# Optimization experiments

Measured on AMD Instinct MI355X. Metric: run time of the kernel, lower is better.

## Reference

```python
import jax, jax.numpy as jnp
import numpy as np

B = 8192        # batch of spots
T = 137         # target_length: number of predict heads
D = 384         # fea_size(256) + img_size(128)
K = 128         # hidden width of each head
EPS = 1e-5      # BatchNorm1d eps
SLOPE = 0.01    # LeakyReLU negative slope (torch default)


def setup_inputs() -> dict:
    key = jax.random.key(0)
    ks = jax.random.split(key, 5)
    return {
        "f":        jax.random.normal(ks[0], (B, D), dtype=jnp.float32),
        "W1":       jax.random.normal(ks[1], (T, K, D), dtype=jnp.float32) * (1.0 / np.sqrt(D)),
        "b1":       jax.random.normal(ks[2], (T, K), dtype=jnp.float32) * 0.02,
        "gamma":    jnp.ones((T, K), dtype=jnp.float32),
        "beta":     jnp.zeros((T, K), dtype=jnp.float32),
        "run_mean": jnp.zeros((T, K), dtype=jnp.float32),
        "run_var":  jnp.ones((T, K), dtype=jnp.float32),
        "W2":       jax.random.normal(ks[3], (T, K), dtype=jnp.float32) * (1.0 / np.sqrt(K)),
        "b2":       jax.random.normal(ks[4], (T,), dtype=jnp.float32) * 0.02,
    }


def reference(f, W1, b1, gamma, beta, run_mean, run_var, W2, b2):
    # Batched equivalent of: for i in range(137): Linear(384->128)+BN+LeakyReLU+Linear(128->1)
    # all applied to the same feature f; outputs concatenated -> [B, 137].
    h = jnp.einsum('bd,tkd->btk', f, W1) + b1                       # [B, T, K]
    scale = gamma * jax.lax.rsqrt(run_var + EPS)                     # eval-mode BN, [T, K]
    h = (h - run_mean) * scale + beta
    h = jnp.where(h >= 0, h, SLOPE * h)                              # LeakyReLU
    out = jnp.einsum('btk,tk->bt', h, W2) + b2                       # [B, T]
    return out
```

## Files before the change

### kernel.cpp

```cpp
#include <hip/hip_runtime.h>
#include <hip/hip_bf16.h>

constexpr int BATCH = 8192;
constexpr int THEADS = 137;
constexpr int DFEA = 384;
constexpr int KHID = 128;
constexpr float EPS_BN = 1e-5f;
constexpr float SLOPE = 0.01f;

constexpr size_t N_F  = (size_t)BATCH * DFEA;
constexpr size_t N_W1 = (size_t)THEADS * KHID * DFEA;
constexpr size_t WS_NEED = (N_F + N_W1) * sizeof(__hip_bfloat16);
constexpr int C_F8 = (int)(N_F / 8);
constexpr int C_T8 = (int)((N_F + N_W1) / 8);

typedef __attribute__((ext_vector_type(8))) short bf16x8;
typedef __attribute__((ext_vector_type(4))) float f32x4;

__device__ __forceinline__ short cvt_bf16(float x) {
    __hip_bfloat16 b = __float2bfloat16(x);
    return *(short*)&b;
}

__device__ __forceinline__ bf16x8 load8_cvt(const float* __restrict__ g) {
    f32x4 lo = *(const f32x4*)g;
    f32x4 hi = *(const f32x4*)(g + 4);
    bf16x8 r;
    r[0] = cvt_bf16(lo[0]); r[1] = cvt_bf16(lo[1]);
    r[2] = cvt_bf16(lo[2]); r[3] = cvt_bf16(lo[3]);
    r[4] = cvt_bf16(hi[0]); r[5] = cvt_bf16(hi[1]);
    r[6] = cvt_bf16(hi[2]); r[7] = cvt_bf16(hi[3]);
    return r;
}

__device__ __forceinline__ void gload16(const void* g, void* s) {
    __builtin_amdgcn_global_load_lds((const __attribute__((address_space(1))) void*)g,
                                     (__attribute__((address_space(3))) void*)s,
                                     16, 0, 0);
}

__global__ __launch_bounds__(256) void cvt_pass(const float* __restrict__ f,
                                                const float* __restrict__ W1,
                                                __hip_bfloat16* __restrict__ ws) {
    int i = blockIdx.x * 256 + threadIdx.x;
    if (i < C_F8)
        *(bf16x8*)(ws + (size_t)i * 8) = load8_cvt(f + (size_t)i * 8);
    else if (i < C_T8)
        *(bf16x8*)(ws + (size_t)i * 8) = load8_cvt(W1 + ((size_t)i - C_F8) * 8);
}

__global__ __launch_bounds__(256, 2) void fused_heads_bf16(
    const __hip_bfloat16* __restrict__ fb,
    const __hip_bfloat16* __restrict__ W1b,
    const float* __restrict__ b1,
    const float* __restrict__ gmm,
    const float* __restrict__ bta,
    const float* __restrict__ rmean,
    const float* __restrict__ rvar,
    const float* __restrict__ W2,
    const float* __restrict__ b2,
    float* __restrict__ out)
{
    __shared__ __attribute__((aligned(16))) __hip_bfloat16 As[256 * 32];
    __shared__ __attribute__((aligned(16))) __hip_bfloat16 Bs[128 * 32];

    const int tid  = threadIdx.x;
    const int lane = tid & 63;
    const int wm   = tid >> 6;
    const int m0 = blockIdx.x * 256;
    const int t  = blockIdx.y;
    const int n0 = t * KHID;

    const int row16 = lane & 15;
    const int quad  = lane >> 4;
    const int swz   = quad ^ ((row16 >> 1) & 3);

    const __hip_bfloat16* gA[4];
    const __hip_bfloat16* gB[2];
    #pragma unroll
    for (int c = 0; c < 4; ++c) {
        const int li = tid + c * 256;
        const int r = li >> 2, cb = (li & 3) ^ ((li >> 3) & 3);
        gA[c] = fb + (size_t)(m0 + r) * DFEA + cb * 8;
    }
    #pragma unroll
    for (int c = 0; c < 2; ++c) {
        const int li = tid + c * 256;
        const int r = li >> 2, cb = (li & 3) ^ ((li >> 3) & 3);
        gB[c] = W1b + (size_t)(n0 + r) * DFEA + cb * 8;
    }

    f32x4 acc[4][8];
    #pragma unroll
    for (int i = 0; i < 4; ++i)
        #pragma unroll
        for (int j = 0; j < 8; ++j)
            acc[i][j] = (f32x4){0.f, 0.f, 0.f, 0.f};

    #pragma unroll 1
    for (int kt = 0; kt < DFEA / 32; ++kt) {
        const int k0 = kt * 32;
        #pragma unroll
        for (int c = 0; c < 4; ++c)
            gload16(gA[c] + k0, &As[(tid + c * 256) * 8]);
        #pragma unroll
        for (int c = 0; c < 2; ++c)
            gload16(gB[c] + k0, &Bs[(tid + c * 256) * 8]);
        __syncthreads();

        bf16x8 af[4], bfr[8];
        #pragma unroll
        for (int ai = 0; ai < 4; ++ai)
            af[ai] = *(const bf16x8*)&As[(wm * 64 + ai * 16 + row16) * 32 + swz * 8];
        #pragma unroll
        for (int bi = 0; bi < 8; ++bi)
            bfr[bi] = *(const bf16x8*)&Bs[(bi * 16 + row16) * 32 + swz * 8];

        #pragma unroll
        for (int ai = 0; ai < 4; ++ai)
            #pragma unroll
            for (int bi = 0; bi < 8; ++bi)
                acc[ai][bi] = __builtin_amdgcn_mfma_f32_16x16x32_bf16(
                    af[ai], bfr[bi], acc[ai][bi], 0, 0, 0);
        __syncthreads();
    }

    float s[8], cc[8], w2v[8];
    #pragma unroll
    for (int bi = 0; bi < 8; ++bi) {
        const int n = n0 + bi * 16 + row16;
        const float sv = gmm[n] * rsqrtf(rvar[n] + EPS_BN);
        s[bi]   = sv;
        cc[bi]  = bta[n] + (b1[n] - rmean[n]) * sv;
        w2v[bi] = W2[n];
    }

    float p[4][4];
    #pragma unroll
    for (int ai = 0; ai < 4; ++ai)
        #pragma unroll
        for (int r = 0; r < 4; ++r) {
            float a = 0.f;
            #pragma unroll
            for (int bi = 0; bi < 8; ++bi) {
                float y = acc[ai][bi][r] * s[bi] + cc[bi];
                y = (y >= 0.f) ? y : SLOPE * y;
                a += y * w2v[bi];
            }
            p[ai][r] = a;
        }

    #pragma unroll
    for (int mask = 1; mask <= 8; mask <<= 1)
        #pragma unroll
        for (int ai = 0; ai < 4; ++ai)
            #pragma unroll
            for (int r = 0; r < 4; ++r)
                p[ai][r] += __shfl_xor(p[ai][r], mask);

    if (row16 == 0) {
        const float bias = b2[t];
        #pragma unroll
        for (int ai = 0; ai < 4; ++ai)
            #pragma unroll
            for (int r = 0; r < 4; ++r) {
                const int row = m0 + wm * 64 + ai * 16 + quad * 4 + r;
                out[(size_t)row * THEADS + t] = p[ai][r] + bias;
            }
    }
}

__global__ __launch_bounds__(256) void fused_heads_f32(
    const float* __restrict__ f, const float* __restrict__ W1,
    const float* __restrict__ b1, const float* __restrict__ gmm,
    const float* __restrict__ bta, const float* __restrict__ rmean,
    const float* __restrict__ rvar, const float* __restrict__ W2,
    const float* __restrict__ b2, float* __restrict__ out)
{
    __shared__ __attribute__((aligned(16))) __hip_bfloat16 As[128 * 32];
    __shared__ __attribute__((aligned(16))) __hip_bfloat16 Bs[128 * 32];
    __shared__ float red[2][128];

    const int tid  = threadIdx.x;
    const int lane = tid & 63;
    const int wave = tid >> 6;
    const int wm = wave >> 1, wn = wave & 1;
    const int m0 = blockIdx.x * 128;
    const int t  = blockIdx.y;
    const int n0 = t * KHID;

    const int li0 = tid, li1 = tid + 256;
    const int r0 = li0 >> 2, c0 = (li0 & 3) * 8;
    const int r1 = li1 >> 2, c1 = (li1 & 3) * 8;
    const float* gA0 = f  + (size_t)(m0 + r0) * DFEA + c0;
    const float* gA1 = f  + (size_t)(m0 + r1) * DFEA + c1;
    const float* gB0 = W1 + (size_t)(n0 + r0) * DFEA + c0;
    const float* gB1 = W1 + (size_t)(n0 + r1) * DFEA + c1;

    const int row16 = lane & 15, quad = lane >> 4;

    f32x4 acc[4][4];
    #pragma unroll
    for (int i = 0; i < 4; ++i)
        #pragma unroll
        for (int j = 0; j < 4; ++j)
            acc[i][j] = (f32x4){0.f, 0.f, 0.f, 0.f};

    #pragma unroll 1
    for (int kt = 0; kt < DFEA / 32; ++kt) {
        const int k0 = kt * 32;
        bf16x8 va0 = load8_cvt(gA0 + k0);
        bf16x8 va1 = load8_cvt(gA1 + k0);
        bf16x8 vb0 = load8_cvt(gB0 + k0);
        bf16x8 vb1 = load8_cvt(gB1 + k0);
        __syncthreads();
        *(bf16x8*)&As[li0 * 8] = va0;
        *(bf16x8*)&As[li1 * 8] = va1;
        *(bf16x8*)&Bs[li0 * 8] = vb0;
        *(bf16x8*)&Bs[li1 * 8] = vb1;
        __syncthreads();

        bf16x8 af[4], bfr[4];
        #pragma unroll
        for (int i = 0; i < 4; ++i)
            af[i] = *(const bf16x8*)&As[(wm * 64 + i * 16 + row16) * 32 + quad * 8];
        #pragma unroll
        for (int i = 0; i < 4; ++i)
            bfr[i] = *(const bf16x8*)&Bs[(wn * 64 + i * 16 + row16) * 32 + quad * 8];
        #pragma unroll
        for (int ai = 0; ai < 4; ++ai)
            #pragma unroll
            for (int bi = 0; bi < 4; ++bi)
                acc[ai][bi] = __builtin_amdgcn_mfma_f32_16x16x32_bf16(
                    af[ai], bfr[bi], acc[ai][bi], 0, 0, 0);
    }

    float s[4], cc[4], w2v[4];
    #pragma unroll
    for (int bi = 0; bi < 4; ++bi) {
        const int n = n0 + wn * 64 + bi * 16 + row16;
        const float sv = gmm[n] * rsqrtf(rvar[n] + EPS_BN);
        s[bi] = sv;
        cc[bi] = bta[n] + (b1[n] - rmean[n]) * sv;
        w2v[bi] = W2[n];
    }
    float p[4][4];
    #pragma unroll
    for (int ai = 0; ai < 4; ++ai)
        #pragma unroll
        for (int r = 0; r < 4; ++r) {
            float a = 0.f;
            #pragma unroll
            for (int bi = 0; bi < 4; ++bi) {
                float y = acc[ai][bi][r] * s[bi] + cc[bi];
                y = (y >= 0.f) ? y : SLOPE * y;
                a += y * w2v[bi];
            }
            p[ai][r] = a;
        }
    #pragma unroll
    for (int mask = 1; mask <= 8; mask <<= 1)
        #pragma unroll
        for (int ai = 0; ai < 4; ++ai)
            #pragma unroll
            for (int r = 0; r < 4; ++r)
                p[ai][r] += __shfl_xor(p[ai][r], mask);
    if (row16 == 0) {
        #pragma unroll
        for (int ai = 0; ai < 4; ++ai)
            #pragma unroll
            for (int r = 0; r < 4; ++r)
                red[wn][wm * 64 + ai * 16 + quad * 4 + r] = p[ai][r];
    }
    __syncthreads();
    if (tid < 128)
        out[(size_t)(m0 + tid) * THEADS + t] = red[0][tid] + red[1][tid] + b2[t];
}

extern "C" void kernel_launch(void* const* d_in, const int* in_sizes, int n_in,
                              void* d_out, int out_size, void* d_ws, size_t ws_size,
                              hipStream_t stream) {
    (void)in_sizes; (void)n_in; (void)out_size;
    const float* f     = (const float*)d_in[0];
    const float* W1    = (const float*)d_in[1];
    const float* b1    = (const float*)d_in[2];
    const float* gmm   = (const float*)d_in[3];
    const float* bta   = (const float*)d_in[4];
    const float* rmean = (const float*)d_in[5];
    const float* rvar  = (const float*)d_in[6];
    const float* W2    = (const float*)d_in[7];
    const float* b2    = (const float*)d_in[8];
    float* out = (float*)d_out;

    if (ws_size >= WS_NEED) {
        __hip_bfloat16* fb  = (__hip_bfloat16*)d_ws;
        __hip_bfloat16* W1b = fb + N_F;
        cvt_pass<<<(C_T8 + 255) / 256, 256, 0, stream>>>(f, W1, fb);
        dim3 grid(BATCH / 256, THEADS);
        fused_heads_bf16<<<grid, 256, 0, stream>>>(fb, W1b, b1, gmm, bta, rmean, rvar, W2, b2, out);
    } else {
        dim3 grid(BATCH / 128, THEADS);
        fused_heads_f32<<<grid, 256, 0, stream>>>(f, W1, b1, gmm, bta, rmean, rvar, W2, b2, out);
    }
}
```

Measured before the change: 222.0 us.

## Restructure bf16 heads kernel: 512-row tiles, direct A loads, double-buffered W1 chunks

The bf16 fused-heads kernel now uses 512-thread blocks covering 512 batch rows per head. The activation fragments are loaded straight from global memory into registers, skipping LDS. Each head's W1 slice is staged in two 128-wide K chunks with an XOR swizzle and double buffering, and the 1D grid is remapped so neighbouring blocks share heads for L2 reuse. The aim is to cut LDS traffic and barriers per K step and to raise MFMA density. The cost is that uncoalesced per-lane global A loads may stall the MFMA pipeline, and the larger LDS footprint (64KB per block) limits occupancy.

New measurement: 244.6 us. 1.1x slower.

```diff
diff --git a/kernel.cpp b/kernel.cpp
--- a/kernel.cpp
+++ b/kernel.cpp
@@ -13,6 +13,9 @@
 constexpr size_t WS_NEED = (N_F + N_W1) * sizeof(__hip_bfloat16);
 constexpr int C_F8 = (int)(N_F / 8);
 constexpr int C_T8 = (int)((N_F + N_W1) / 8);
+
+constexpr int BM   = 512;
+constexpr int NBLK = (BATCH / BM) * THEADS;
 
 typedef __attribute__((ext_vector_type(8))) short bf16x8;
 typedef __attribute__((ext_vector_type(4))) float f32x4;
@@ -49,7 +52,7 @@
         *(bf16x8*)(ws + (size_t)i * 8) = load8_cvt(W1 + ((size_t)i - C_F8) * 8);
 }
 
-__global__ __launch_bounds__(256, 2) void fused_heads_bf16(
+__global__ __launch_bounds__(512, 2) void fused_heads_v2(
     const __hip_bfloat16* __restrict__ fb,
     const __hip_bfloat16* __restrict__ W1b,
     const float* __restrict__ b1,
@@ -61,76 +64,93 @@
     const float* __restrict__ b2,
     float* __restrict__ out)
 {
-    __shared__ __attribute__((aligned(16))) __hip_bfloat16 As[256 * 32];
-    __shared__ __attribute__((aligned(16))) __hip_bfloat16 Bs[128 * 32];
-
-    const int tid  = threadIdx.x;
-    const int lane = tid & 63;
-    const int wm   = tid >> 6;
-    const int m0 = blockIdx.x * 256;
-    const int t  = blockIdx.y;
-    const int n0 = t * KHID;
-
+    __shared__ __attribute__((aligned(16))) __hip_bfloat16 Bs[2][KHID * 128];
+
+    const int tid   = threadIdx.x;
+    const int lane  = tid & 63;
+    const int wm    = tid >> 6;
     const int row16 = lane & 15;
     const int quad  = lane >> 4;
-    const int swz   = quad ^ ((row16 >> 1) & 3);
+
+    const int bid  = blockIdx.x;
+    const int j    = bid >> 3;
+    const int mblk = ((bid & 7) << 1) | (j & 1);
+    const int t    = j >> 1;
+    const int m0   = mblk * BM;
+    const int n0   = t * KHID;
+
+    const __hip_bfloat16* gB[4];
+    int ldst[4];
+    #pragma unroll
+    for (int jj = 0; jj < 4; ++jj) {
+        const int li = tid + jj * 512;
+        const int r = li >> 4, s = li & 15;
+        gB[jj]   = W1b + (size_t)(n0 + r) * DFEA + ((s ^ (r & 7)) << 3);
+        ldst[jj] = li << 3;
+    }
 
     const __hip_bfloat16* gA[4];
-    const __hip_bfloat16* gB[2];
-    #pragma unroll
-    for (int c = 0; c < 4; ++c) {
-        const int li = tid + c * 256;
-        const int r = li >> 2, cb = (li & 3) ^ ((li >> 3) & 3);
-        gA[c] = fb + (size_t)(m0 + r) * DFEA + cb * 8;
-    }
-    #pragma unroll
-    for (int c = 0; c < 2; ++c) {
-        const int li = tid + c * 256;
-        const int r = li >> 2, cb = (li & 3) ^ ((li >> 3) & 3);
-        gB[c] = W1b + (size_t)(n0 + r) * DFEA + cb * 8;
-    }
+    #pragma unroll
+    for (int ai = 0; ai < 4; ++ai)
+        gA[ai] = fb + (size_t)(m0 + wm * 64 + ai * 16 + row16) * DFEA + quad * 8;
 
     f32x4 acc[4][8];
     #pragma unroll
     for (int i = 0; i < 4; ++i)
         #pragma unroll
-        for (int j = 0; j < 8; ++j)
-            acc[i][j] = (f32x4){0.f, 0.f, 0.f, 0.f};
-
-    #pragma unroll 1
-    for (int kt = 0; kt < DFEA / 32; ++kt) {
-        const int k0 = kt * 32;
-        #pragma unroll
-        for (int c = 0; c < 4; ++c)
-            gload16(gA[c] + k0, &As[(tid + c * 256) * 8]);
-        #pragma unroll
-        for (int c = 0; c < 2; ++c)
-            gload16(gB[c] + k0, &Bs[(tid + c * 256) * 8]);
-        __syncthreads();
-
-        bf16x8 af[4], bfr[8];
-        #pragma unroll
-        for (int ai = 0; ai < 4; ++ai)
-            af[ai] = *(const bf16x8*)&As[(wm * 64 + ai * 16 + row16) * 32 + swz * 8];
-        #pragma unroll
-        for (int bi = 0; bi < 8; ++bi)
-            bfr[bi] = *(const bf16x8*)&Bs[(bi * 16 + row16) * 32 + swz * 8];
-
-        #pragma unroll
-        for (int ai = 0; ai < 4; ++ai)
-            #pragma unroll
-            for (int bi = 0; bi < 8; ++bi)
-                acc[ai][bi] = __builtin_amdgcn_mfma_f32_16x16x32_bf16(
-                    af[ai], bfr[bi], acc[ai][bi], 0, 0, 0);
-        __syncthreads();
-    }
-
-    float s[8], cc[8], w2v[8];
+        for (int jx = 0; jx < 8; ++jx)
+            acc[i][jx] = (f32x4){0.f, 0.f, 0.f, 0.f};
+
+    #pragma unroll
+    for (int jj = 0; jj < 4; ++jj) gload16(gB[jj],       &Bs[0][ldst[jj]]);
+    #pragma unroll
+    for (int jj = 0; jj < 4; ++jj) gload16(gB[jj] + 128, &Bs[1][ldst[jj]]);
+
+    bf16x8 af0[4];
+    #pragma unroll
+    for (int ai = 0; ai < 4; ++ai) af0[ai] = *(const bf16x8*)gA[ai];
+
+    __syncthreads();
+
+#define CHUNK(BUF, C, PRE)                                                   \
+    {                                                                        \
+        _Pragma("unroll")                                                    \
+        for (int ktl = 0; ktl < 4; ++ktl) {                                  \
+            bf16x8 af[4], bfr[8];                                            \
+            _Pragma("unroll")                                                \
+            for (int ai = 0; ai < 4; ++ai)                                   \
+                af[ai] = ((PRE) && ktl == 0) ? af0[ai]                       \
+                       : *(const bf16x8*)(gA[ai] + (C) * 128 + ktl * 32);    \
+            _Pragma("unroll")                                                \
+            for (int bi = 0; bi < 8; ++bi) {                                 \
+                const int rr = bi * 16 + row16;                              \
+                const int ss = (ktl * 4 + quad) ^ (row16 & 7);               \
+                bfr[bi] = *(const bf16x8*)&Bs[BUF][rr * 128 + ss * 8];       \
+            }                                                                \
+            _Pragma("unroll")                                                \
+            for (int ai = 0; ai < 4; ++ai)                                   \
+                _Pragma("unroll")                                            \
+                for (int bi = 0; bi < 8; ++bi)                               \
+                    acc[ai][bi] = __builtin_amdgcn_mfma_f32_16x16x32_bf16(   \
+                        af[ai], bfr[bi], acc[ai][bi], 0, 0, 0);              \
+        }                                                                    \
+    }
+
+    CHUNK(0, 0, true)
+    __syncthreads();
+    #pragma unroll
+    for (int jj = 0; jj < 4; ++jj) gload16(gB[jj] + 256, &Bs[0][ldst[jj]]);
+    CHUNK(1, 1, false)
+    __syncthreads();
+    CHUNK(0, 2, false)
+#undef CHUNK
+
+    float sc[8], cc[8], w2v[8];
     #pragma unroll
     for (int bi = 0; bi < 8; ++bi) {
         const int n = n0 + bi * 16 + row16;
         const float sv = gmm[n] * rsqrtf(rvar[n] + EPS_BN);
-        s[bi]   = sv;
+        sc[bi]  = sv;
         cc[bi]  = bta[n] + (b1[n] - rmean[n]) * sv;
         w2v[bi] = W2[n];
     }
@@ -143,7 +163,7 @@
             float a = 0.f;
             #pragma unroll
             for (int bi = 0; bi < 8; ++bi) {
-                float y = acc[ai][bi][r] * s[bi] + cc[bi];
+                float y = acc[ai][bi][r] * sc[bi] + cc[bi];
                 y = (y >= 0.f) ? y : SLOPE * y;
                 a += y * w2v[bi];
             }
@@ -184,7 +204,7 @@
     const int tid  = threadIdx.x;
     const int lane = tid & 63;
     const int wave = tid >> 6;
-    const int wm = wave >> 1, wn = wave & 1;
+    const int wmv = wave >> 1, wn = wave & 1;
     const int m0 = blockIdx.x * 128;
     const int t  = blockIdx.y;
     const int n0 = t * KHID;
@@ -203,8 +223,8 @@
     #pragma unroll
     for (int i = 0; i < 4; ++i)
         #pragma unroll
-        for (int j = 0; j < 4; ++j)
-            acc[i][j] = (f32x4){0.f, 0.f, 0.f, 0.f};
+        for (int jx = 0; jx < 4; ++jx)
+            acc[i][jx] = (f32x4){0.f, 0.f, 0.f, 0.f};
 
     #pragma unroll 1
     for (int kt = 0; kt < DFEA / 32; ++kt) {
@@ -223,7 +243,7 @@
         bf16x8 af[4], bfr[4];
         #pragma unroll
         for (int i = 0; i < 4; ++i)
-            af[i] = *(const bf16x8*)&As[(wm * 64 + i * 16 + row16) * 32 + quad * 8];
+            af[i] = *(const bf16x8*)&As[(wmv * 64 + i * 16 + row16) * 32 + quad * 8];
         #pragma unroll
         for (int i = 0; i < 4; ++i)
             bfr[i] = *(const bf16x8*)&Bs[(wn * 64 + i * 16 + row16) * 32 + quad * 8];
@@ -270,7 +290,7 @@
         for (int ai = 0; ai < 4; ++ai)
             #pragma unroll
             for (int r = 0; r < 4; ++r)
-                red[wn][wm * 64 + ai * 16 + quad * 4 + r] = p[ai][r];
+                red[wn][wmv * 64 + ai * 16 + quad * 4 + r] = p[ai][r];
     }
     __syncthreads();
     if (tid < 128)
@@ -296,8 +316,7 @@
         __hip_bfloat16* fb  = (__hip_bfloat16*)d_ws;
         __hip_bfloat16* W1b = fb + N_F;
         cvt_pass<<<(C_T8 + 255) / 256, 256, 0, stream>>>(f, W1, fb);
-        dim3 grid(BATCH / 256, THEADS);
-        fused_heads_bf16<<<grid, 256, 0, stream>>>(fb, W1b, b1, gmm, bta, rmean, rvar, W2, b2, out);
+        fused_heads_v2<<<dim3(NBLK), 512, 0, stream>>>(fb, W1b, b1, gmm, bta, rmean, rvar, W2, b2, out);
     } else {
         dim3 grid(BATCH / 128, THEADS);
         fused_heads_f32<<<grid, 256, 0, stream>>>(f, W1, b1, gmm, bta, rmean, rvar, W2, b2, out);
```

## Double-buffer LDS tiles with async prefetch of next K-slice in bf16 kernel

Applied to the files above, without the earlier changes.

The bf16 GEMM loop now uses two LDS buffers for A and B. It issues the global-to-LDS loads for the next K tile before computing on the current one, and uses explicit vmcnt waits and raw barriers instead of two __syncthreads per iteration. This is meant to hide global load latency behind the MFMA work and to cut barrier stalls. It also raises wave priority around the MFMA block. LDS use doubles to 48KB per block, which may limit occupancy at 2 blocks per CU, and the hand-written waitcnt counts must match the number of loads issued.

Result: no change. 223.1 us (+0.5%).

```diff
diff --git a/kernel.cpp b/kernel.cpp
--- a/kernel.cpp
+++ b/kernel.cpp
@@ -49,7 +49,7 @@
         *(bf16x8*)(ws + (size_t)i * 8) = load8_cvt(W1 + ((size_t)i - C_F8) * 8);
 }
 
-__global__ __launch_bounds__(256, 2) void fused_heads_bf16(
+__global__ __launch_bounds__(256, 2) void fused_heads_v5(
     const __hip_bfloat16* __restrict__ fb,
     const __hip_bfloat16* __restrict__ W1b,
     const float* __restrict__ b1,
@@ -61,8 +61,8 @@
     const float* __restrict__ b2,
     float* __restrict__ out)
 {
-    __shared__ __attribute__((aligned(16))) __hip_bfloat16 As[256 * 32];
-    __shared__ __attribute__((aligned(16))) __hip_bfloat16 Bs[128 * 32];
+    __shared__ __attribute__((aligned(16))) __hip_bfloat16 As[2][256 * 32];
+    __shared__ __attribute__((aligned(16))) __hip_bfloat16 Bs[2][128 * 32];
 
     const int tid  = threadIdx.x;
     const int lane = tid & 63;
@@ -97,33 +97,50 @@
         for (int j = 0; j < 8; ++j)
             acc[i][j] = (f32x4){0.f, 0.f, 0.f, 0.f};
 
-    #pragma unroll 1
+#define STAGE(BUF, K0)                                                      \
+    {                                                                       \
+        _Pragma("unroll")                                                   \
+        for (int c = 0; c < 4; ++c)                                         \
+            gload16(gA[c] + (K0), &As[BUF][(tid + c * 256) * 8]);           \
+        _Pragma("unroll")                                                   \
+        for (int c = 0; c < 2; ++c)                                         \
+            gload16(gB[c] + (K0), &Bs[BUF][(tid + c * 256) * 8]);           \
+    }
+
+    STAGE(0, 0);
+
+    #pragma unroll 2
     for (int kt = 0; kt < DFEA / 32; ++kt) {
-        const int k0 = kt * 32;
-        #pragma unroll
-        for (int c = 0; c < 4; ++c)
-            gload16(gA[c] + k0, &As[(tid + c * 256) * 8]);
-        #pragma unroll
-        for (int c = 0; c < 2; ++c)
-            gload16(gB[c] + k0, &Bs[(tid + c * 256) * 8]);
-        __syncthreads();
+        const int cur = kt & 1;
+        if (kt < 11) {
+            STAGE(cur ^ 1, (kt + 1) * 32);
+            asm volatile("s_waitcnt vmcnt(6)" ::: "memory");
+        } else {
+            asm volatile("s_waitcnt vmcnt(0)" ::: "memory");
+        }
+        __builtin_amdgcn_s_barrier();
+        __builtin_amdgcn_sched_barrier(0);
 
         bf16x8 af[4], bfr[8];
         #pragma unroll
         for (int ai = 0; ai < 4; ++ai)
-            af[ai] = *(const bf16x8*)&As[(wm * 64 + ai * 16 + row16) * 32 + swz * 8];
+            af[ai] = *(const bf16x8*)&As[cur][(wm * 64 + ai * 16 + row16) * 32 + swz * 8];
         #pragma unroll
         for (int bi = 0; bi < 8; ++bi)
-            bfr[bi] = *(const bf16x8*)&Bs[(bi * 16 + row16) * 32 + swz * 8];
-
+            bfr[bi] = *(const bf16x8*)&Bs[cur][(bi * 16 + row16) * 32 + swz * 8];
+
+        __builtin_amdgcn_s_setprio(1);
         #pragma unroll
         for (int ai = 0; ai < 4; ++ai)
             #pragma unroll
             for (int bi = 0; bi < 8; ++bi)
                 acc[ai][bi] = __builtin_amdgcn_mfma_f32_16x16x32_bf16(
                     af[ai], bfr[bi], acc[ai][bi], 0, 0, 0);
-        __syncthreads();
-    }
+        __builtin_amdgcn_s_setprio(0);
+
+        __builtin_amdgcn_s_barrier();
+    }
+#undef STAGE
 
     float s[8], cc[8], w2v[8];
     #pragma unroll
@@ -184,7 +201,7 @@
     const int tid  = threadIdx.x;
     const int lane = tid & 63;
     const int wave = tid >> 6;
-    const int wm = wave >> 1, wn = wave & 1;
+    const int wmv = wave >> 1, wn = wave & 1;
     const int m0 = blockIdx.x * 128;
     const int t  = blockIdx.y;
     const int n0 = t * KHID;
@@ -203,8 +220,8 @@
     #pragma unroll
     for (int i = 0; i < 4; ++i)
         #pragma unroll
-        for (int j = 0; j < 4; ++j)
-            acc[i][j] = (f32x4){0.f, 0.f, 0.f, 0.f};
+        for (int jx = 0; jx < 4; ++jx)
+            acc[i][jx] = (f32x4){0.f, 0.f, 0.f, 0.f};
 
     #pragma unroll 1
     for (int kt = 0; kt < DFEA / 32; ++kt) {
@@ -223,7 +240,7 @@
         bf16x8 af[4], bfr[4];
         #pragma unroll
         for (int i = 0; i < 4; ++i)
-            af[i] = *(const bf16x8*)&As[(wm * 64 + i * 16 + row16) * 32 + quad * 8];
+            af[i] = *(const bf16x8*)&As[(wmv * 64 + i * 16 + row16) * 32 + quad * 8];
         #pragma unroll
         for (int i = 0; i < 4; ++i)
             bfr[i] = *(const bf16x8*)&Bs[(wn * 64 + i * 16 + row16) * 32 + quad * 8];
@@ -270,7 +287,7 @@
         for (int ai = 0; ai < 4; ++ai)
             #pragma unroll
             for (int r = 0; r < 4; ++r)
-                red[wn][wm * 64 + ai * 16 + quad * 4 + r] = p[ai][r];
+                red[wn][wmv * 64 + ai * 16 + quad * 4 + r] = p[ai][r];
     }
     __syncthreads();
     if (tid < 128)
@@ -297,7 +314,7 @@
         __hip_bfloat16* W1b = fb + N_F;
         cvt_pass<<<(C_T8 + 255) / 256, 256, 0, stream>>>(f, W1, fb);
         dim3 grid(BATCH / 256, THEADS);
-        fused_heads_bf16<<<grid, 256, 0, stream>>>(fb, W1b, b1, gmm, bta, rmean, rvar, W2, b2, out);
+        fused_heads_v5<<<grid, 256, 0, stream>>>(fb, W1b, b1, gmm, bta, rmean, rvar, W2, b2, out);
     } else {
         dim3 grid(BATCH / 128, THEADS);
         fused_heads_f32<<<grid, 256, 0, stream>>>(f, W1, b1, gmm, bta, rmean, rvar, W2, b2, out);
```

## Load MFMA operands directly from global into registers with double buffering

Applied to the files above, without the earlier changes.

The bf16 GEMM kernel no longer stages A and B tiles through LDS with global_load_lds and two barriers per k-step. Each wave now loads its MFMA fragments straight from global memory into registers, double-buffered across two k-slices in a fully unrolled loop. MFMA blocks run at raised wave priority via s_setprio. This removes LDS traffic and block-wide syncs, but each wave fetches the whole B tile on its own (4x redundant B reads served by cache) and register pressure rises from the two fragment buffers.

Result: slower. 388.5 us (+75.0%).

```diff
diff --git a/kernel.cpp b/kernel.cpp
--- a/kernel.cpp
+++ b/kernel.cpp
@@ -33,12 +33,6 @@
     return r;
 }
 
-__device__ __forceinline__ void gload16(const void* g, void* s) {
-    __builtin_amdgcn_global_load_lds((const __attribute__((address_space(1))) void*)g,
-                                     (__attribute__((address_space(3))) void*)s,
-                                     16, 0, 0);
-}
-
 __global__ __launch_bounds__(256) void cvt_pass(const float* __restrict__ f,
                                                 const float* __restrict__ W1,
                                                 __hip_bfloat16* __restrict__ ws) {
@@ -49,7 +43,7 @@
         *(bf16x8*)(ws + (size_t)i * 8) = load8_cvt(W1 + ((size_t)i - C_F8) * 8);
 }
 
-__global__ __launch_bounds__(256, 2) void fused_heads_bf16(
+__global__ __launch_bounds__(256, 2) void fused_heads_v6(
     const __hip_bfloat16* __restrict__ fb,
     const __hip_bfloat16* __restrict__ W1b,
     const float* __restrict__ b1,
@@ -61,34 +55,51 @@
     const float* __restrict__ b2,
     float* __restrict__ out)
 {
-    __shared__ __attribute__((aligned(16))) __hip_bfloat16 As[256 * 32];
-    __shared__ __attribute__((aligned(16))) __hip_bfloat16 Bs[128 * 32];
-
-    const int tid  = threadIdx.x;
-    const int lane = tid & 63;
-    const int wm   = tid >> 6;
+    const int tid   = threadIdx.x;
+    const int lane  = tid & 63;
+    const int wm    = tid >> 6;
+    const int row16 = lane & 15;
+    const int quad  = lane >> 4;
     const int m0 = blockIdx.x * 256;
     const int t  = blockIdx.y;
     const int n0 = t * KHID;
 
-    const int row16 = lane & 15;
-    const int quad  = lane >> 4;
-    const int swz   = quad ^ ((row16 >> 1) & 3);
-
-    const __hip_bfloat16* gA[4];
-    const __hip_bfloat16* gB[2];
-    #pragma unroll
-    for (int c = 0; c < 4; ++c) {
-        const int li = tid + c * 256;
-        const int r = li >> 2, cb = (li & 3) ^ ((li >> 3) & 3);
-        gA[c] = fb + (size_t)(m0 + r) * DFEA + cb * 8;
-    }
-    #pragma unroll
-    for (int c = 0; c < 2; ++c) {
-        const int li = tid + c * 256;
-        const int r = li >> 2, cb = (li & 3) ^ ((li >> 3) & 3);
-        gB[c] = W1b + (size_t)(n0 + r) * DFEA + cb * 8;
-    }
+    const int laneoff = row16 * DFEA + quad * 8;
+
+    const __hip_bfloat16* aB[4];
+    #pragma unroll
+    for (int ai = 0; ai < 4; ++ai)
+        aB[ai] = fb + (size_t)__builtin_amdgcn_readfirstlane((m0 + wm * 64 + ai * 16) * DFEA)
+                    + laneoff;
+    const __hip_bfloat16* bB[8];
+    #pragma unroll
+    for (int bi = 0; bi < 8; ++bi)
+        bB[bi] = W1b + (size_t)__builtin_amdgcn_readfirstlane((n0 + bi * 16) * DFEA)
+                     + laneoff;
+
+#define LOADA(dst, K)                                                 \
+    { _Pragma("unroll")                                               \
+      for (int ai = 0; ai < 4; ++ai)                                  \
+          dst[ai] = *(const bf16x8*)(aB[ai] + (K) * 32); }
+
+#define LOADB(dst, K)                                                 \
+    { _Pragma("unroll")                                               \
+      for (int bi = 0; bi < 8; ++bi)                                  \
+          dst[bi] = *(const bf16x8*)(bB[bi] + (K) * 32); }
+
+#define MFMA32(AF, BF)                                                \
+    { __builtin_amdgcn_s_setprio(1);                                  \
+      _Pragma("unroll")                                               \
+      for (int ai = 0; ai < 4; ++ai)                                  \
+          _Pragma("unroll")                                           \
+          for (int bi = 0; bi < 8; ++bi)                              \
+              acc[ai][bi] = __builtin_amdgcn_mfma_f32_16x16x32_bf16(  \
+                  AF[ai], BF[bi], acc[ai][bi], 0, 0, 0);              \
+      __builtin_amdgcn_s_setprio(0); }
+
+    bf16x8 afa[4], bfa[8], afb[4], bfb[8];
+    LOADA(afa, 0); LOADB(bfa, 0);
+    LOADA(afb, 1); LOADB(bfb, 1);
 
     f32x4 acc[4][8];
     #pragma unroll
@@ -97,33 +108,16 @@
         for (int j = 0; j < 8; ++j)
             acc[i][j] = (f32x4){0.f, 0.f, 0.f, 0.f};
 
-    #pragma unroll 1
-    for (int kt = 0; kt < DFEA / 32; ++kt) {
-        const int k0 = kt * 32;
-        #pragma unroll
-        for (int c = 0; c < 4; ++c)
-            gload16(gA[c] + k0, &As[(tid + c * 256) * 8]);
-        #pragma unroll
-        for (int c = 0; c < 2; ++c)
-            gload16(gB[c] + k0, &Bs[(tid + c * 256) * 8]);
-        __syncthreads();
-
-        bf16x8 af[4], bfr[8];
-        #pragma unroll
-        for (int ai = 0; ai < 4; ++ai)
-            af[ai] = *(const bf16x8*)&As[(wm * 64 + ai * 16 + row16) * 32 + swz * 8];
-        #pragma unroll
-        for (int bi = 0; bi < 8; ++bi)
-            bfr[bi] = *(const bf16x8*)&Bs[(bi * 16 + row16) * 32 + swz * 8];
-
-        #pragma unroll
-        for (int ai = 0; ai < 4; ++ai)
-            #pragma unroll
-            for (int bi = 0; bi < 8; ++bi)
-                acc[ai][bi] = __builtin_amdgcn_mfma_f32_16x16x32_bf16(
-                    af[ai], bfr[bi], acc[ai][bi], 0, 0, 0);
-        __syncthreads();
-    }
+    #pragma unroll
+    for (int kp = 0; kp < 6; ++kp) {
+        MFMA32(afa, bfa);
+        if (kp < 5) { LOADA(afa, 2 * kp + 2); LOADB(bfa, 2 * kp + 2); }
+        MFMA32(afb, bfb);
+        if (kp < 5) { LOADA(afb, 2 * kp + 3); LOADB(bfb, 2 * kp + 3); }
+    }
+#undef LOADA
+#undef LOADB
+#undef MFMA32
 
     float s[8], cc[8], w2v[8];
     #pragma unroll
@@ -184,7 +178,7 @@
     const int tid  = threadIdx.x;
     const int lane = tid & 63;
     const int wave = tid >> 6;
-    const int wm = wave >> 1, wn = wave & 1;
+    const int wmv = wave >> 1, wn = wave & 1;
     const int m0 = blockIdx.x * 128;
     const int t  = blockIdx.y;
     const int n0 = t * KHID;
@@ -203,8 +197,8 @@
     #pragma unroll
     for (int i = 0; i < 4; ++i)
         #pragma unroll
-        for (int j = 0; j < 4; ++j)
-            acc[i][j] = (f32x4){0.f, 0.f, 0.f, 0.f};
+        for (int jx = 0; jx < 4; ++jx)
+            acc[i][jx] = (f32x4){0.f, 0.f, 0.f, 0.f};
 
     #pragma unroll 1
     for (int kt = 0; kt < DFEA / 32; ++kt) {
@@ -223,7 +217,7 @@
         bf16x8 af[4], bfr[4];
         #pragma unroll
         for (int i = 0; i < 4; ++i)
-            af[i] = *(const bf16x8*)&As[(wm * 64 + i * 16 + row16) * 32 + quad * 8];
+            af[i] = *(const bf16x8*)&As[(wmv * 64 + i * 16 + row16) * 32 + quad * 8];
         #pragma unroll
         for (int i = 0; i < 4; ++i)
             bfr[i] = *(const bf16x8*)&Bs[(wn * 64 + i * 16 + row16) * 32 + quad * 8];
@@ -270,7 +264,7 @@
         for (int ai = 0; ai < 4; ++ai)
             #pragma unroll
             for (int r = 0; r < 4; ++r)
-                red[wn][wm * 64 + ai * 16 + quad * 4 + r] = p[ai][r];
+                red[wn][wmv * 64 + ai * 16 + quad * 4 + r] = p[ai][r];
     }
     __syncthreads();
     if (tid < 128)
@@ -297,7 +291,7 @@
         __hip_bfloat16* W1b = fb + N_F;
         cvt_pass<<<(C_T8 + 255) / 256, 256, 0, stream>>>(f, W1, fb);
         dim3 grid(BATCH / 256, THEADS);
-        fused_heads_bf16<<<grid, 256, 0, stream>>>(fb, W1b, b1, gmm, bta, rmean, rvar, W2, b2, out);
+        fused_heads_v6<<<grid, 256, 0, stream>>>(fb, W1b, b1, gmm, bta, rmean, rvar, W2, b2, out);
     } else {
         dim3 grid(BATCH / 128, THEADS);
         fused_heads_f32<<<grid, 256, 0, stream>>>(f, W1, b1, gmm, bta, rmean, rvar, W2, b2, out);
```
